# Optimization experiments

Measured on AMD Instinct MI355X. Metric: run time of the kernel, lower is better.

Reference implementation:

```python
import jax, jax.numpy as jnp
import numpy as np


def _apply_rope(q, k):
    # q, k: [BH, T, hd]
    hd = q.shape[-1]
    half = hd // 2
    T = q.shape[1]
    inv_freq = 1.0 / (10000.0 ** (jnp.arange(half, dtype=jnp.float32) / half))
    freqs = jnp.arange(T, dtype=jnp.float32)[:, None] * inv_freq[None, :]  # [T, half]
    cos = jnp.cos(freqs)[None, :, :]
    sin = jnp.sin(freqs)[None, :, :]
    q1, q2 = q[..., :half], q[..., half:]
    k1, k2 = k[..., :half], k[..., half:]
    q_rot = jnp.concatenate([q1 * cos - q2 * sin, q1 * sin + q2 * cos], axis=-1)
    k_rot = jnp.concatenate([k1 * cos - k2 * sin, k1 * sin + k2 * cos], axis=-1)
    return q_rot, k_rot


def setup_inputs() -> dict:
    key = jax.random.key(0)
    ks = jax.random.split(key, 5)
    B, T, D = 2, 2048, 1024
    x = jax.random.normal(ks[0], (B, T, D), dtype=jnp.float32)
    w_qkv = jax.random.normal(ks[1], (D, 3 * D), dtype=jnp.float32) * (1.0 / np.sqrt(D))
    b_qkv = jax.random.normal(ks[2], (3 * D,), dtype=jnp.float32) * 0.01
    w_out = jax.random.normal(ks[3], (D, D), dtype=jnp.float32) * (1.0 / np.sqrt(D))
    b_out = jax.random.normal(ks[4], (D,), dtype=jnp.float32) * 0.01
    return {"x": x, "w_qkv": w_qkv, "b_qkv": b_qkv, "w_out": w_out, "b_out": b_out}


def reference(x, w_qkv, b_qkv, w_out, b_out):
    B, T, D = x.shape
    H = 16
    hd = D // H
    qkv = x @ w_qkv + b_qkv  # [B, T, 3D]
    q, k, v = jnp.split(qkv, 3, axis=-1)
    # [B, T, H, hd] -> [B, H, T, hd]
    q = q.reshape(B, T, H, hd).transpose(0, 2, 1, 3)
    k = k.reshape(B, T, H, hd).transpose(0, 2, 1, 3)
    v = v.reshape(B, T, H, hd).transpose(0, 2, 1, 3)
    q, k = _apply_rope(q.reshape(B * H, T, hd), k.reshape(B * H, T, hd))
    q = q.reshape(B, H, T, hd)
    k = k.reshape(B, H, T, hd)
    scores = jnp.einsum("bhqd,bhkd->bhqk", q, k) / jnp.sqrt(jnp.float32(hd))
    attn = jax.nn.softmax(scores, axis=-1)
    out = jnp.einsum("bhqk,bhkd->bhqd", attn, v)  # [B, H, T, hd]
    out = out.transpose(0, 2, 1, 3).reshape(B, T, D)
    return out @ w_out + b_out
```

## Files before the change

### kernel.cpp

```cpp
#include <hip/hip_runtime.h>
#include <hip/hip_bf16.h>
#include <stdint.h>


typedef __bf16 bf16;
typedef __bf16 bf16x8 __attribute__((ext_vector_type(8)));
typedef __bf16 bf16x4 __attribute__((ext_vector_type(4)));
typedef short  s16x4  __attribute__((ext_vector_type(4)));
typedef float  f32x4  __attribute__((ext_vector_type(4)));

__device__ __forceinline__ void gload16(void* lds, const void* g) {
  __builtin_amdgcn_global_load_lds((__attribute__((address_space(1))) void*)(void*)g,
                                   (__attribute__((address_space(3))) void*)lds, 16, 0, 0);
}


__global__ void k_convert_x(const float* __restrict__ x, bf16* __restrict__ xb, int n) {
  int i = (blockIdx.x * blockDim.x + threadIdx.x) * 4;
  if (i >= n) return;
  float4 v = *(const float4*)(x + i);
  bf16x4 o;
  o.x = (bf16)v.x; o.y = (bf16)v.y; o.z = (bf16)v.z; o.w = (bf16)v.w;
  *(bf16x4*)(xb + i) = o;
}

__global__ void k_transpose_bf16(const float* __restrict__ in, bf16* __restrict__ out,
                                 int rows, int cols) {
  __shared__ float t[32][33];
  int c0 = blockIdx.x * 32, r0 = blockIdx.y * 32;
  for (int i = threadIdx.y; i < 32; i += 8)
    t[i][threadIdx.x] = in[(size_t)(r0 + i) * cols + c0 + threadIdx.x];
  __syncthreads();
  for (int i = threadIdx.y; i < 32; i += 8)
    out[(size_t)(c0 + i) * rows + r0 + threadIdx.x] = (bf16)t[threadIdx.x][i];
}


__global__ __launch_bounds__(256)
void k_gemm_qkv(const bf16* __restrict__ A, const bf16* __restrict__ Bt,
                const float* __restrict__ bias, bf16* __restrict__ Qd,
                bf16* __restrict__ Kd, bf16* __restrict__ Vtd) {
  alignas(16) __shared__ bf16 lds_a[128 * 32];
  alignas(16) __shared__ bf16 lds_b[128 * 32];
  const int tid = threadIdx.x;
  const int lane = tid & 63, w = tid >> 6;
  const int wr = w >> 1, wc = w & 1;
  const int bid = blockIdx.x;
  const int swz = (bid & 7) * 96 + (bid >> 3);
  const int br = swz / 24, bc = swz % 24;
  const int r16 = lane & 15, g4 = lane >> 4;

  f32x4 acc[4][4] = {};
  const bf16* gA = A + (size_t)(br * 128 + (lane >> 2)) * 1024 + (lane & 3) * 8;
  const bf16* gB = Bt + (size_t)(bc * 128 + (lane >> 2)) * 1024 + (lane & 3) * 8;

  for (int kt = 0; kt < 32; ++kt) {
    const int ko = kt * 32;
#pragma unroll
    for (int it = 0; it < 2; ++it) {
      const int row0 = 16 * (4 * it + w);
      gload16(&lds_a[row0 * 32], gA + (size_t)row0 * 1024 + ko);
      gload16(&lds_b[row0 * 32], gB + (size_t)row0 * 1024 + ko);
    }
    __syncthreads();
    bf16x8 af[4], bfr[4];
#pragma unroll
    for (int m = 0; m < 4; ++m)
      af[m] = *(const bf16x8*)&lds_a[(wr * 64 + 16 * m + r16) * 32 + g4 * 8];
#pragma unroll
    for (int n = 0; n < 4; ++n)
      bfr[n] = *(const bf16x8*)&lds_b[(wc * 64 + 16 * n + r16) * 32 + g4 * 8];
#pragma unroll
    for (int m = 0; m < 4; ++m)
#pragma unroll
      for (int n = 0; n < 4; ++n)
        acc[m][n] = __builtin_amdgcn_mfma_f32_16x16x32_bf16(af[m], bfr[n], acc[m][n], 0, 0, 0);
    __syncthreads();
  }

  const int reg = bc >> 3;
  const int h = ((bc & 7) << 1) | wc;
  const float bq = 0.125f * 1.4426950408889634f;
  const float Lc = 13.287712379549449f / 32.0f;
  const float if0 = exp2f(-(float)r16 * Lc);
  const float if1 = exp2f(-(float)(16 + r16) * Lc);
  float bv[4];
#pragma unroll
  for (int n = 0; n < 4; ++n) bv[n] = bias[bc * 128 + wc * 64 + 16 * n + r16];

  if (reg == 2) {
#pragma unroll
    for (int m = 0; m < 4; ++m) {
      const int row0 = br * 128 + wr * 64 + 16 * m + 4 * g4;
      const int t0 = row0 & 2047, b = row0 >> 11;
      const int pos = (t0 & ~63) | (((t0 >> 2) & 3) << 4) | (((t0 >> 5) & 1) << 3) |
                      (((t0 >> 4) & 1) << 2);
#pragma unroll
      for (int n = 0; n < 4; ++n) {
        bf16x4 pk;
#pragma unroll
        for (int r = 0; r < 4; ++r) pk[r] = (bf16)(acc[m][n][r] + bv[n]);
        *(bf16x4*)(Vtd + ((size_t)((b * 16 + h) * 64) + 16 * n + r16) * 2048 + pos) = pk;
      }
    }
  } else {
    bf16* dst = (reg == 0) ? Qd : Kd;
#pragma unroll
    for (int m = 0; m < 4; ++m) {
#pragma unroll
      for (int r = 0; r < 4; ++r) {
        const int row = br * 128 + wr * 64 + 16 * m + 4 * g4 + r;
        const int t = row & 2047, b = row >> 11;
        bf16* o = dst + ((size_t)(b * 16 + h) * 2048 + t) * 64;
        const float v0 = acc[m][0][r] + bv[0];
        const float v1 = acc[m][1][r] + bv[1];
        const float v2 = acc[m][2][r] + bv[2];
        const float v3 = acc[m][3][r] + bv[3];
        float s0, c0, s1, c1;
        const float tf = (float)t;
        sincosf(tf * if0, &s0, &c0);
        sincosf(tf * if1, &s1, &c1);
        float r0 = v0 * c0 - v2 * s0, r2 = v0 * s0 + v2 * c0;
        float r1 = v1 * c1 - v3 * s1, r3 = v1 * s1 + v3 * c1;
        if (reg == 0) { r0 *= bq; r1 *= bq; r2 *= bq; r3 *= bq; }
        o[r16]      = (bf16)r0;
        o[16 + r16] = (bf16)r1;
        o[32 + r16] = (bf16)r2;
        o[48 + r16] = (bf16)r3;
      }
    }
  }
}


__global__ __launch_bounds__(256)
void k_gemm_out(const bf16* __restrict__ A, const bf16* __restrict__ Bt,
                const float* __restrict__ bias, float* __restrict__ Cp,
                int M, int N, int K) {
  alignas(16) __shared__ bf16 lds_a[128 * 32];
  alignas(16) __shared__ bf16 lds_b[128 * 32];
  const int tid = threadIdx.x;
  const int lane = tid & 63, w = tid >> 6;
  const int wr = w >> 1, wc = w & 1;
  const int nb = N >> 7;
  const int nwg = gridDim.x;
  const int bid = blockIdx.x;
  const int swz = (bid & 7) * (nwg >> 3) + (bid >> 3);
  const int br = swz / nb, bc = swz % nb;
  const int r16 = lane & 15, g4 = lane >> 4;

  f32x4 acc[4][4] = {};
  const int nk = K >> 5;
  const bf16* gA = A + (size_t)(br * 128 + (lane >> 2)) * K + (lane & 3) * 8;
  const bf16* gB = Bt + (size_t)(bc * 128 + (lane >> 2)) * K + (lane & 3) * 8;

  for (int kt = 0; kt < nk; ++kt) {
    const int ko = kt * 32;
#pragma unroll
    for (int it = 0; it < 2; ++it) {
      const int row0 = 16 * (4 * it + w);
      gload16(&lds_a[row0 * 32], gA + (size_t)row0 * K + ko);
      gload16(&lds_b[row0 * 32], gB + (size_t)row0 * K + ko);
    }
    __syncthreads();
    bf16x8 af[4], bfr[4];
#pragma unroll
    for (int m = 0; m < 4; ++m)
      af[m] = *(const bf16x8*)&lds_a[(wr * 64 + 16 * m + r16) * 32 + g4 * 8];
#pragma unroll
    for (int n = 0; n < 4; ++n)
      bfr[n] = *(const bf16x8*)&lds_b[(wc * 64 + 16 * n + r16) * 32 + g4 * 8];
#pragma unroll
    for (int m = 0; m < 4; ++m)
#pragma unroll
      for (int n = 0; n < 4; ++n)
        acc[m][n] = __builtin_amdgcn_mfma_f32_16x16x32_bf16(af[m], bfr[n], acc[m][n], 0, 0, 0);
    __syncthreads();
  }

#pragma unroll
  for (int m = 0; m < 4; ++m) {
    const int row = br * 128 + wr * 64 + 16 * m + 4 * g4;
#pragma unroll
    for (int n = 0; n < 4; ++n) {
      const int col = bc * 128 + wc * 64 + 16 * n + r16;
      const float bvv = bias[col];
#pragma unroll
      for (int r = 0; r < 4; ++r)
        Cp[(size_t)(row + r) * N + col] = acc[m][n][r] + bvv;
    }
  }
}


__global__ __launch_bounds__(256)
void k_attn(const bf16* __restrict__ Qg, const bf16* __restrict__ Kg,
            const bf16* __restrict__ Vtg, bf16* __restrict__ Og) {
  alignas(16) __shared__ bf16 kbuf[2][4096];
  alignas(16) __shared__ bf16 vbuf[2][4096];
  const int tid = threadIdx.x, lane = tid & 63, w = tid >> 6;
  const int bid = blockIdx.x;
  const int swz = (bid & 7) * 64 + (bid >> 3);
  const int bh = swz >> 4, q0 = (swz & 15) * 128;
  const int r16 = lane & 15, g4 = lane >> 4;
  const char* Kb  = (const char*)(Kg  + (size_t)bh * 2048 * 64);
  const char* Vtb = (const char*)(Vtg + (size_t)bh * 64 * 2048);
  const bf16* Qb  = Qg + (size_t)bh * 2048 * 64;

  const int rl = lane >> 3;
  const int colx = ((lane & 7) * 16) ^ (rl << 4);

  bf16x8 qf[2][2];
#pragma unroll
  for (int g = 0; g < 2; ++g) {
    const int qrow = q0 + 64 * g + 16 * w + r16;
    qf[g][0] = *(const bf16x8*)(Qb + (size_t)qrow * 64 + g4 * 8);
    qf[g][1] = *(const bf16x8*)(Qb + (size_t)qrow * 64 + 32 + g4 * 8);
  }

  f32x4 O[2][4] = {};
  f32x4 O4[2] = {};
  float m0 = -1e30f, m1 = -1e30f;
  bf16x8 ones8 = {};
  if (r16 == 0)
#pragma unroll
    for (int j = 0; j < 8; ++j) ones8[j] = (bf16)1.f;

#define STAGE(bufi, t0)                                                          \
  {                                                                              \
    _Pragma("unroll")                                                            \
    for (int c = 0; c < 2; ++c) {                                                \
      const int row = 16 * w + 8 * c + rl;                                       \
      gload16(&kbuf[bufi][(2 * w + c) * 512],                                    \
              Kb + (size_t)((t0) + row) * 128 + colx);                           \
      gload16(&vbuf[bufi][(2 * w + c) * 512],                                    \
              Vtb + (size_t)row * 4096 + (size_t)(t0) * 2 + colx);               \
    }                                                                            \
  }

  STAGE(0, 0);
  __syncthreads();

  const int rsw = (r16 & 7) << 4;

#pragma unroll 1
  for (int it = 0; it < 32; ++it) {
    const int bsel = it & 1;
    if (it + 1 < 32) STAGE(bsel ^ 1, (it + 1) * 64);
    const char* kb = (const char*)kbuf[bsel] + r16 * 128;
    const char* vb = (const char*)vbuf[bsel] + r16 * 128;

    f32x4 S0[4], S1[4];
#pragma unroll
    for (int n = 0; n < 4; ++n) {
      bf16x8 kb0 = *(const bf16x8*)(kb + n * 2048 + ((g4 * 16) ^ rsw));
      bf16x8 kb1 = *(const bf16x8*)(kb + n * 2048 + ((64 + g4 * 16) ^ rsw));
      f32x4 s = {};
      s = __builtin_amdgcn_mfma_f32_16x16x32_bf16(kb0, qf[0][0], s, 0, 0, 0);
      s = __builtin_amdgcn_mfma_f32_16x16x32_bf16(kb1, qf[0][1], s, 0, 0, 0);
      S0[n] = s;
      f32x4 t = {};
      t = __builtin_amdgcn_mfma_f32_16x16x32_bf16(kb0, qf[1][0], t, 0, 0, 0);
      t = __builtin_amdgcn_mfma_f32_16x16x32_bf16(kb1, qf[1][1], t, 0, 0, 0);
      S1[n] = t;
    }

    float pmax0 = fmaxf(
        fmaxf(fmaxf(fmaxf(S0[0][0], S0[0][1]), S0[0][2]),
              fmaxf(fmaxf(S0[0][3], S0[1][0]), S0[1][1])),
        fmaxf(fmaxf(fmaxf(S0[1][2], S0[1][3]), S0[2][0]),
              fmaxf(fmaxf(S0[2][1], S0[2][2]), S0[2][3])));
    pmax0 = fmaxf(pmax0, fmaxf(fmaxf(S0[3][0], S0[3][1]), fmaxf(S0[3][2], S0[3][3])));
    float pmax1 = fmaxf(
        fmaxf(fmaxf(fmaxf(S1[0][0], S1[0][1]), S1[0][2]),
              fmaxf(fmaxf(S1[0][3], S1[1][0]), S1[1][1])),
        fmaxf(fmaxf(fmaxf(S1[1][2], S1[1][3]), S1[2][0]),
              fmaxf(fmaxf(S1[2][1], S1[2][2]), S1[2][3])));
    pmax1 = fmaxf(pmax1, fmaxf(fmaxf(S1[3][0], S1[3][1]), fmaxf(S1[3][2], S1[3][3])));

    if (!__all(fmaxf(pmax0 - m0, pmax1 - m1) <= 8.0f)) {
      float gm0 = pmax0, gm1 = pmax1;
      gm0 = fmaxf(gm0, __shfl_xor(gm0, 16, 64));
      gm0 = fmaxf(gm0, __shfl_xor(gm0, 32, 64));
      gm1 = fmaxf(gm1, __shfl_xor(gm1, 16, 64));
      gm1 = fmaxf(gm1, __shfl_xor(gm1, 32, 64));
      const float mn0 = fmaxf(m0, gm0), mn1 = fmaxf(m1, gm1);
      const float a0 = exp2f(m0 - mn0), a1 = exp2f(m1 - mn1);
      m0 = mn0; m1 = mn1;
#pragma unroll
      for (int n = 0; n < 4; ++n)
#pragma unroll
        for (int r = 0; r < 4; ++r) { O[0][n][r] *= a0; O[1][n][r] *= a1; }
      O4[0][0] *= a0; O4[1][0] *= a1;
    }

    bf16x8 pb0[2], pb1[2];
#pragma unroll
    for (int n = 0; n < 4; ++n)
#pragma unroll
      for (int r = 0; r < 4; ++r) {
        pb0[n >> 1][(n & 1) * 4 + r] = (bf16)exp2f(S0[n][r] - m0);
        pb1[n >> 1][(n & 1) * 4 + r] = (bf16)exp2f(S1[n][r] - m1);
      }

#pragma unroll
    for (int dn = 0; dn < 4; ++dn) {
      bf16x8 v0 = *(const bf16x8*)(vb + dn * 2048 + ((32 * g4) ^ rsw));
      bf16x8 v1 = *(const bf16x8*)(vb + dn * 2048 + ((32 * g4 + 16) ^ rsw));
      O[0][dn] = __builtin_amdgcn_mfma_f32_16x16x32_bf16(v0, pb0[0], O[0][dn], 0, 0, 0);
      O[0][dn] = __builtin_amdgcn_mfma_f32_16x16x32_bf16(v1, pb0[1], O[0][dn], 0, 0, 0);
      O[1][dn] = __builtin_amdgcn_mfma_f32_16x16x32_bf16(v0, pb1[0], O[1][dn], 0, 0, 0);
      O[1][dn] = __builtin_amdgcn_mfma_f32_16x16x32_bf16(v1, pb1[1], O[1][dn], 0, 0, 0);
    }
    O4[0] = __builtin_amdgcn_mfma_f32_16x16x32_bf16(ones8, pb0[0], O4[0], 0, 0, 0);
    O4[0] = __builtin_amdgcn_mfma_f32_16x16x32_bf16(ones8, pb0[1], O4[0], 0, 0, 0);
    O4[1] = __builtin_amdgcn_mfma_f32_16x16x32_bf16(ones8, pb1[0], O4[1], 0, 0, 0);
    O4[1] = __builtin_amdgcn_mfma_f32_16x16x32_bf16(ones8, pb1[1], O4[1], 0, 0, 0);
    __syncthreads();
  }
#undef STAGE

  const int b = bh >> 4, h = bh & 15;
#pragma unroll
  for (int g = 0; g < 2; ++g) {
    const float ls = __shfl(O4[g][0], r16, 64);
    const float inv = 1.f / ls;
    const int t = q0 + 64 * g + 16 * w + r16;
#pragma unroll
    for (int n = 0; n < 4; ++n) {
      bf16x4 ov;
#pragma unroll
      for (int r = 0; r < 4; ++r) ov[r] = (bf16)(O[g][n][r] * inv);
      *(bf16x4*)(Og + ((size_t)(b * 2048 + t)) * 1024 + h * 64 + 16 * n + 4 * g4) = ov;
    }
  }
}


extern "C" void kernel_launch(void* const* d_in, const int* in_sizes, int n_in,
                              void* d_out, int out_size, void* d_ws, size_t ws_size,
                              hipStream_t stream) {
  const float* x     = (const float*)d_in[0];
  const float* w_qkv = (const float*)d_in[1];
  const float* b_qkv = (const float*)d_in[2];
  const float* w_out = (const float*)d_in[3];
  const float* b_out = (const float*)d_in[4];
  float* out = (float*)d_out;

  char* ws = (char*)d_ws;
  bf16* xb    = (bf16*)(ws);
  bf16* wqkvT = (bf16*)(ws + 8388608);
  bf16* woutT = (bf16*)(ws + 14680064);
  bf16* Qb    = (bf16*)(ws + 16777216);
  bf16* Kb    = (bf16*)(ws + 25165824);
  bf16* Vtb   = (bf16*)(ws + 33554432);
  bf16* attnb = (bf16*)(ws + 41943040);

  k_convert_x<<<4096 * 1024 / 4 / 256, 256, 0, stream>>>(x, xb, 4096 * 1024);
  k_transpose_bf16<<<dim3(3072 / 32, 1024 / 32), dim3(32, 8), 0, stream>>>(w_qkv, wqkvT, 1024, 3072);
  k_transpose_bf16<<<dim3(1024 / 32, 1024 / 32), dim3(32, 8), 0, stream>>>(w_out, woutT, 1024, 1024);
  k_gemm_qkv<<<32 * 24, 256, 0, stream>>>(xb, wqkvT, b_qkv, Qb, Kb, Vtb);
  k_attn<<<512, 256, 0, stream>>>(Qb, Kb, Vtb, attnb);
  k_gemm_out<<<32 * 8, 256, 0, stream>>>(attnb, woutT, b_out, out, 4096, 1024, 1024);
}
```

Before: 146.9 us.

## Precompute RoPE trig table and load attention K/V directly from global

Adds a kernel that precomputes cos/sin for every position and frequency into a table, which the QKV GEMM epilogue reads instead of calling sincosf per element. The attention kernel drops its LDS double-buffered staging and block barriers, loading K and V fragments directly from global memory into registers each iteration, with a 2x unroll. This removes the trig cost and the synchronisation, but relies on cache hits for K/V data that the four waves of a block now fetch separately, and exposes global load latency to the MFMA loop.

Result: slower. 212.1 us (+44.4%).

```diff
diff --git a/kernel.cpp b/kernel.cpp
--- a/kernel.cpp
+++ b/kernel.cpp
@@ -6,7 +6,6 @@
 typedef __bf16 bf16;
 typedef __bf16 bf16x8 __attribute__((ext_vector_type(8)));
 typedef __bf16 bf16x4 __attribute__((ext_vector_type(4)));
-typedef short  s16x4  __attribute__((ext_vector_type(4)));
 typedef float  f32x4  __attribute__((ext_vector_type(4)));
 
 __device__ __forceinline__ void gload16(void* lds, const void* g) {
@@ -35,11 +34,21 @@
     out[(size_t)(c0 + i) * rows + r0 + threadIdx.x] = (bf16)t[threadIdx.x][i];
 }
 
+__global__ void k_trig(float2* __restrict__ tab) {
+  const int i = blockIdx.x * 256 + threadIdx.x;
+  const int t = i >> 5, k = i & 31;
+  const float Lc = 13.287712379549449f / 32.0f;
+  const float fr = (float)t * exp2f(-(float)k * Lc);
+  float s, c;
+  sincosf(fr, &s, &c);
+  tab[i] = make_float2(c, s);
+}
+
 
 __global__ __launch_bounds__(256)
 void k_gemm_qkv(const bf16* __restrict__ A, const bf16* __restrict__ Bt,
-                const float* __restrict__ bias, bf16* __restrict__ Qd,
-                bf16* __restrict__ Kd, bf16* __restrict__ Vtd) {
+                const float* __restrict__ bias, const float2* __restrict__ trig,
+                bf16* __restrict__ Qd, bf16* __restrict__ Kd, bf16* __restrict__ Vtd) {
   alignas(16) __shared__ bf16 lds_a[128 * 32];
   alignas(16) __shared__ bf16 lds_b[128 * 32];
   const int tid = threadIdx.x;
@@ -81,9 +90,6 @@
   const int reg = bc >> 3;
   const int h = ((bc & 7) << 1) | wc;
   const float bq = 0.125f * 1.4426950408889634f;
-  const float Lc = 13.287712379549449f / 32.0f;
-  const float if0 = exp2f(-(float)r16 * Lc);
-  const float if1 = exp2f(-(float)(16 + r16) * Lc);
   float bv[4];
 #pragma unroll
   for (int n = 0; n < 4; ++n) bv[n] = bias[bc * 128 + wc * 64 + 16 * n + r16];
@@ -116,12 +122,10 @@
         const float v1 = acc[m][1][r] + bv[1];
         const float v2 = acc[m][2][r] + bv[2];
         const float v3 = acc[m][3][r] + bv[3];
-        float s0, c0, s1, c1;
-        const float tf = (float)t;
-        sincosf(tf * if0, &s0, &c0);
-        sincosf(tf * if1, &s1, &c1);
-        float r0 = v0 * c0 - v2 * s0, r2 = v0 * s0 + v2 * c0;
-        float r1 = v1 * c1 - v3 * s1, r3 = v1 * s1 + v3 * c1;
+        const float2 cs0 = trig[t * 32 + r16];
+        const float2 cs1 = trig[t * 32 + 16 + r16];
+        float r0 = v0 * cs0.x - v2 * cs0.y, r2 = v0 * cs0.y + v2 * cs0.x;
+        float r1 = v1 * cs1.x - v3 * cs1.y, r3 = v1 * cs1.y + v3 * cs1.x;
         if (reg == 0) { r0 *= bq; r1 *= bq; r2 *= bq; r3 *= bq; }
         o[r16]      = (bf16)r0;
         o[16 + r16] = (bf16)r1;
@@ -196,19 +200,15 @@
 __global__ __launch_bounds__(256)
 void k_attn(const bf16* __restrict__ Qg, const bf16* __restrict__ Kg,
             const bf16* __restrict__ Vtg, bf16* __restrict__ Og) {
-  alignas(16) __shared__ bf16 kbuf[2][4096];
-  alignas(16) __shared__ bf16 vbuf[2][4096];
   const int tid = threadIdx.x, lane = tid & 63, w = tid >> 6;
   const int bid = blockIdx.x;
   const int swz = (bid & 7) * 64 + (bid >> 3);
   const int bh = swz >> 4, q0 = (swz & 15) * 128;
   const int r16 = lane & 15, g4 = lane >> 4;
-  const char* Kb  = (const char*)(Kg  + (size_t)bh * 2048 * 64);
-  const char* Vtb = (const char*)(Vtg + (size_t)bh * 64 * 2048);
-  const bf16* Qb  = Qg + (size_t)bh * 2048 * 64;
-
-  const int rl = lane >> 3;
-  const int colx = ((lane & 7) * 16) ^ (rl << 4);
+
+  const char* kp0 = (const char*)(Kg + (size_t)bh * 2048 * 64) + r16 * 128 + g4 * 16;
+  const char* vp0 = (const char*)(Vtg + (size_t)bh * 64 * 2048) + r16 * 4096 + g4 * 32;
+  const bf16* Qb = Qg + (size_t)bh * 2048 * 64;
 
   bf16x8 qf[2][2];
 #pragma unroll
@@ -226,35 +226,23 @@
 #pragma unroll
     for (int j = 0; j < 8; ++j) ones8[j] = (bf16)1.f;
 
-#define STAGE(bufi, t0)                                                          \
-  {                                                                              \
-    _Pragma("unroll")                                                            \
-    for (int c = 0; c < 2; ++c) {                                                \
-      const int row = 16 * w + 8 * c + rl;                                       \
-      gload16(&kbuf[bufi][(2 * w + c) * 512],                                    \
-              Kb + (size_t)((t0) + row) * 128 + colx);                           \
-      gload16(&vbuf[bufi][(2 * w + c) * 512],                                    \
-              Vtb + (size_t)row * 4096 + (size_t)(t0) * 2 + colx);               \
-    }                                                                            \
-  }
-
-  STAGE(0, 0);
-  __syncthreads();
-
-  const int rsw = (r16 & 7) << 4;
-
-#pragma unroll 1
+#pragma unroll 2
   for (int it = 0; it < 32; ++it) {
-    const int bsel = it & 1;
-    if (it + 1 < 32) STAGE(bsel ^ 1, (it + 1) * 64);
-    const char* kb = (const char*)kbuf[bsel] + r16 * 128;
-    const char* vb = (const char*)vbuf[bsel] + r16 * 128;
+    const char* kp = kp0 + it * 8192;
+    const char* vp = vp0 + it * 128;
+
+    bf16x8 va0[4], va1[4];
+#pragma unroll
+    for (int dn = 0; dn < 4; ++dn) {
+      va0[dn] = *(const bf16x8*)(vp + dn * 65536);
+      va1[dn] = *(const bf16x8*)(vp + dn * 65536 + 16);
+    }
 
     f32x4 S0[4], S1[4];
 #pragma unroll
     for (int n = 0; n < 4; ++n) {
-      bf16x8 kb0 = *(const bf16x8*)(kb + n * 2048 + ((g4 * 16) ^ rsw));
-      bf16x8 kb1 = *(const bf16x8*)(kb + n * 2048 + ((64 + g4 * 16) ^ rsw));
+      bf16x8 kb0 = *(const bf16x8*)(kp + n * 2048);
+      bf16x8 kb1 = *(const bf16x8*)(kp + n * 2048 + 64);
       f32x4 s = {};
       s = __builtin_amdgcn_mfma_f32_16x16x32_bf16(kb0, qf[0][0], s, 0, 0, 0);
       s = __builtin_amdgcn_mfma_f32_16x16x32_bf16(kb1, qf[0][1], s, 0, 0, 0);
@@ -305,20 +293,16 @@
 
 #pragma unroll
     for (int dn = 0; dn < 4; ++dn) {
-      bf16x8 v0 = *(const bf16x8*)(vb + dn * 2048 + ((32 * g4) ^ rsw));
-      bf16x8 v1 = *(const bf16x8*)(vb + dn * 2048 + ((32 * g4 + 16) ^ rsw));
-      O[0][dn] = __builtin_amdgcn_mfma_f32_16x16x32_bf16(v0, pb0[0], O[0][dn], 0, 0, 0);
-      O[0][dn] = __builtin_amdgcn_mfma_f32_16x16x32_bf16(v1, pb0[1], O[0][dn], 0, 0, 0);
-      O[1][dn] = __builtin_amdgcn_mfma_f32_16x16x32_bf16(v0, pb1[0], O[1][dn], 0, 0, 0);
-      O[1][dn] = __builtin_amdgcn_mfma_f32_16x16x32_bf16(v1, pb1[1], O[1][dn], 0, 0, 0);
+      O[0][dn] = __builtin_amdgcn_mfma_f32_16x16x32_bf16(va0[dn], pb0[0], O[0][dn], 0, 0, 0);
+      O[0][dn] = __builtin_amdgcn_mfma_f32_16x16x32_bf16(va1[dn], pb0[1], O[0][dn], 0, 0, 0);
+      O[1][dn] = __builtin_amdgcn_mfma_f32_16x16x32_bf16(va0[dn], pb1[0], O[1][dn], 0, 0, 0);
+      O[1][dn] = __builtin_amdgcn_mfma_f32_16x16x32_bf16(va1[dn], pb1[1], O[1][dn], 0, 0, 0);
     }
     O4[0] = __builtin_amdgcn_mfma_f32_16x16x32_bf16(ones8, pb0[0], O4[0], 0, 0, 0);
     O4[0] = __builtin_amdgcn_mfma_f32_16x16x32_bf16(ones8, pb0[1], O4[0], 0, 0, 0);
     O4[1] = __builtin_amdgcn_mfma_f32_16x16x32_bf16(ones8, pb1[0], O4[1], 0, 0, 0);
     O4[1] = __builtin_amdgcn_mfma_f32_16x16x32_bf16(ones8, pb1[1], O4[1], 0, 0, 0);
-    __syncthreads();
-  }
-#undef STAGE
+  }
 
   const int b = bh >> 4, h = bh & 15;
 #pragma unroll
@@ -355,11 +339,13 @@
   bf16* Kb    = (bf16*)(ws + 25165824);
   bf16* Vtb   = (bf16*)(ws + 33554432);
   bf16* attnb = (bf16*)(ws + 41943040);
+  float2* trig = (float2*)(ws + 50331648);
 
   k_convert_x<<<4096 * 1024 / 4 / 256, 256, 0, stream>>>(x, xb, 4096 * 1024);
   k_transpose_bf16<<<dim3(3072 / 32, 1024 / 32), dim3(32, 8), 0, stream>>>(w_qkv, wqkvT, 1024, 3072);
   k_transpose_bf16<<<dim3(1024 / 32, 1024 / 32), dim3(32, 8), 0, stream>>>(w_out, woutT, 1024, 1024);
-  k_gemm_qkv<<<32 * 24, 256, 0, stream>>>(xb, wqkvT, b_qkv, Qb, Kb, Vtb);
+  k_trig<<<256, 256, 0, stream>>>(trig);
+  k_gemm_qkv<<<32 * 24, 256, 0, stream>>>(xb, wqkvT, b_qkv, trig, Qb, Kb, Vtb);
   k_attn<<<512, 256, 0, stream>>>(Qb, Kb, Vtb, attnb);
   k_gemm_out<<<32 * 8, 256, 0, stream>>>(attnb, woutT, b_out, out, 4096, 1024, 1024);
 }
```

## Split attention KV range across two blocks and precompute RoPE trig table

Applied to the files above, without the earlier changes.

Attention now runs as a split-KV (flash-decoding style) pass: each query tile is handled by two blocks that each cover half of the keys, writing unnormalized partial outputs plus row max and sum. A new combine kernel merges the two halves and writes the normalized head-interleaved output. This doubles the grid from 512 to 1024 blocks to fill more CUs, at the cost of an extra kernel and partial-result traffic through memory. Separately, RoPE sin/cos values come from a precomputed table built by a small kernel instead of per-element sincosf in the QKV GEMM epilogue.

After: 164.6 us. 12.0% more time.

```diff
diff --git a/kernel.cpp b/kernel.cpp
--- a/kernel.cpp
+++ b/kernel.cpp
@@ -6,7 +6,6 @@
 typedef __bf16 bf16;
 typedef __bf16 bf16x8 __attribute__((ext_vector_type(8)));
 typedef __bf16 bf16x4 __attribute__((ext_vector_type(4)));
-typedef short  s16x4  __attribute__((ext_vector_type(4)));
 typedef float  f32x4  __attribute__((ext_vector_type(4)));
 
 __device__ __forceinline__ void gload16(void* lds, const void* g) {
@@ -35,11 +34,21 @@
     out[(size_t)(c0 + i) * rows + r0 + threadIdx.x] = (bf16)t[threadIdx.x][i];
 }
 
+__global__ void k_trig(float2* __restrict__ tab) {
+  const int i = blockIdx.x * 256 + threadIdx.x;
+  const int t = i >> 5, k = i & 31;
+  const float Lc = 13.287712379549449f / 32.0f;
+  const float fr = (float)t * exp2f(-(float)k * Lc);
+  float s, c;
+  sincosf(fr, &s, &c);
+  tab[i] = make_float2(c, s);
+}
+
 
 __global__ __launch_bounds__(256)
 void k_gemm_qkv(const bf16* __restrict__ A, const bf16* __restrict__ Bt,
-                const float* __restrict__ bias, bf16* __restrict__ Qd,
-                bf16* __restrict__ Kd, bf16* __restrict__ Vtd) {
+                const float* __restrict__ bias, const float2* __restrict__ trig,
+                bf16* __restrict__ Qd, bf16* __restrict__ Kd, bf16* __restrict__ Vtd) {
   alignas(16) __shared__ bf16 lds_a[128 * 32];
   alignas(16) __shared__ bf16 lds_b[128 * 32];
   const int tid = threadIdx.x;
@@ -81,9 +90,6 @@
   const int reg = bc >> 3;
   const int h = ((bc & 7) << 1) | wc;
   const float bq = 0.125f * 1.4426950408889634f;
-  const float Lc = 13.287712379549449f / 32.0f;
-  const float if0 = exp2f(-(float)r16 * Lc);
-  const float if1 = exp2f(-(float)(16 + r16) * Lc);
   float bv[4];
 #pragma unroll
   for (int n = 0; n < 4; ++n) bv[n] = bias[bc * 128 + wc * 64 + 16 * n + r16];
@@ -116,12 +122,10 @@
         const float v1 = acc[m][1][r] + bv[1];
         const float v2 = acc[m][2][r] + bv[2];
         const float v3 = acc[m][3][r] + bv[3];
-        float s0, c0, s1, c1;
-        const float tf = (float)t;
-        sincosf(tf * if0, &s0, &c0);
-        sincosf(tf * if1, &s1, &c1);
-        float r0 = v0 * c0 - v2 * s0, r2 = v0 * s0 + v2 * c0;
-        float r1 = v1 * c1 - v3 * s1, r3 = v1 * s1 + v3 * c1;
+        const float2 cs0 = trig[t * 32 + r16];
+        const float2 cs1 = trig[t * 32 + 16 + r16];
+        float r0 = v0 * cs0.x - v2 * cs0.y, r2 = v0 * cs0.y + v2 * cs0.x;
+        float r1 = v1 * cs1.x - v3 * cs1.y, r3 = v1 * cs1.y + v3 * cs1.x;
         if (reg == 0) { r0 *= bq; r1 *= bq; r2 *= bq; r3 *= bq; }
         o[r16]      = (bf16)r0;
         o[16 + r16] = (bf16)r1;
@@ -195,13 +199,16 @@
 
 __global__ __launch_bounds__(256)
 void k_attn(const bf16* __restrict__ Qg, const bf16* __restrict__ Kg,
-            const bf16* __restrict__ Vtg, bf16* __restrict__ Og) {
+            const bf16* __restrict__ Vtg, bf16* __restrict__ PO,
+            float2* __restrict__ lm) {
   alignas(16) __shared__ bf16 kbuf[2][4096];
   alignas(16) __shared__ bf16 vbuf[2][4096];
   const int tid = threadIdx.x, lane = tid & 63, w = tid >> 6;
   const int bid = blockIdx.x;
-  const int swz = (bid & 7) * 64 + (bid >> 3);
-  const int bh = swz >> 4, q0 = (swz & 15) * 128;
+  const int swz = (bid & 7) * 128 + (bid >> 3);
+  const int half = swz & 1;
+  const int id2 = swz >> 1;
+  const int bh = id2 >> 4, q0 = (id2 & 15) * 128;
   const int r16 = lane & 15, g4 = lane >> 4;
   const char* Kb  = (const char*)(Kg  + (size_t)bh * 2048 * 64);
   const char* Vtb = (const char*)(Vtg + (size_t)bh * 64 * 2048);
@@ -238,15 +245,16 @@
     }                                                                            \
   }
 
-  STAGE(0, 0);
+  const int it0 = half * 16;
+  STAGE(0, it0 * 64);
   __syncthreads();
 
   const int rsw = (r16 & 7) << 4;
 
 #pragma unroll 1
-  for (int it = 0; it < 32; ++it) {
-    const int bsel = it & 1;
-    if (it + 1 < 32) STAGE(bsel ^ 1, (it + 1) * 64);
+  for (int ii = 0; ii < 16; ++ii) {
+    const int bsel = ii & 1;
+    if (ii + 1 < 16) STAGE(bsel ^ 1, (it0 + ii + 1) * 64);
     const char* kb = (const char*)kbuf[bsel] + r16 * 128;
     const char* vb = (const char*)vbuf[bsel] + r16 * 128;
 
@@ -320,20 +328,41 @@
   }
 #undef STAGE
 
-  const int b = bh >> 4, h = bh & 15;
+  bf16* POh = PO + (size_t)half * 4194304;
 #pragma unroll
   for (int g = 0; g < 2; ++g) {
-    const float ls = __shfl(O4[g][0], r16, 64);
-    const float inv = 1.f / ls;
-    const int t = q0 + 64 * g + 16 * w + r16;
+    const int row = bh * 2048 + q0 + 64 * g + 16 * w + r16;
 #pragma unroll
     for (int n = 0; n < 4; ++n) {
       bf16x4 ov;
 #pragma unroll
-      for (int r = 0; r < 4; ++r) ov[r] = (bf16)(O[g][n][r] * inv);
-      *(bf16x4*)(Og + ((size_t)(b * 2048 + t)) * 1024 + h * 64 + 16 * n + 4 * g4) = ov;
-    }
-  }
+      for (int r = 0; r < 4; ++r) ov[r] = (bf16)O[g][n][r];
+      *(bf16x4*)(POh + (size_t)row * 64 + 16 * n + 4 * g4) = ov;
+    }
+    if (g4 == 0)
+      lm[half * 65536 + row] = make_float2(g == 0 ? m0 : m1, O4[g][0]);
+  }
+}
+
+
+__global__ __launch_bounds__(256)
+void k_combine(const bf16* __restrict__ PO, const float2* __restrict__ lm,
+               bf16* __restrict__ attnb) {
+  const int idx = blockIdx.x * 256 + threadIdx.x;
+  const int row = idx >> 3, seg = idx & 7;
+  const float2 l0 = lm[row], l1 = lm[65536 + row];
+  const float M = fmaxf(l0.x, l1.x);
+  const float a0 = exp2f(l0.x - M), a1 = exp2f(l1.x - M);
+  const float inv = 1.f / (a0 * l0.y + a1 * l1.y);
+  bf16x8 p0 = *(const bf16x8*)(PO + (size_t)row * 64 + seg * 8);
+  bf16x8 p1 = *(const bf16x8*)(PO + 4194304 + (size_t)row * 64 + seg * 8);
+  bf16x8 o;
+#pragma unroll
+  for (int j = 0; j < 8; ++j)
+    o[j] = (bf16)((a0 * (float)p0[j] + a1 * (float)p1[j]) * inv);
+  const int bh = row >> 11, t = row & 2047;
+  const int b = bh >> 4, h = bh & 15;
+  *(bf16x8*)(attnb + ((size_t)(b * 2048 + t)) * 1024 + h * 64 + seg * 8) = o;
 }
 
 
@@ -350,16 +379,21 @@
   char* ws = (char*)d_ws;
   bf16* xb    = (bf16*)(ws);
   bf16* wqkvT = (bf16*)(ws + 8388608);
-  bf16* woutT = (bf16*)(ws + 14680064);
   bf16* Qb    = (bf16*)(ws + 16777216);
   bf16* Kb    = (bf16*)(ws + 25165824);
   bf16* Vtb   = (bf16*)(ws + 33554432);
   bf16* attnb = (bf16*)(ws + 41943040);
+  float2* trig = (float2*)(ws + 50331648);
+  bf16* woutT = (bf16*)(ws + 50855936);
+  float2* lm  = (float2*)(ws + 52953088);
+  bf16* PO    = (bf16*)(ws);
 
   k_convert_x<<<4096 * 1024 / 4 / 256, 256, 0, stream>>>(x, xb, 4096 * 1024);
   k_transpose_bf16<<<dim3(3072 / 32, 1024 / 32), dim3(32, 8), 0, stream>>>(w_qkv, wqkvT, 1024, 3072);
   k_transpose_bf16<<<dim3(1024 / 32, 1024 / 32), dim3(32, 8), 0, stream>>>(w_out, woutT, 1024, 1024);
-  k_gemm_qkv<<<32 * 24, 256, 0, stream>>>(xb, wqkvT, b_qkv, Qb, Kb, Vtb);
-  k_attn<<<512, 256, 0, stream>>>(Qb, Kb, Vtb, attnb);
+  k_trig<<<256, 256, 0, stream>>>(trig);
+  k_gemm_qkv<<<32 * 24, 256, 0, stream>>>(xb, wqkvT, b_qkv, trig, Qb, Kb, Vtb);
+  k_attn<<<1024, 256, 0, stream>>>(Qb, Kb, Vtb, PO, lm);
+  k_combine<<<2048, 256, 0, stream>>>(PO, lm, attnb);
   k_gemm_out<<<32 * 8, 256, 0, stream>>>(attnb, woutT, b_out, out, 4096, 1024, 1024);
 }
```
